# Optimization experiments

Hardware: AMD Instinct MI355X
Metric: run time of the kernel (lower is better)

Reference implementation:

```python
import jax, jax.numpy as jnp
import numpy as np

B, T, D, R, V, L, QK, H = 8, 1024, 768, 768, 768, 13, 32, 4
HEAD_DIM = QK // H  # 8
TEMPERATURE = 2.0
LN_EPS = 1e-5


def _layernorm(x, g, b):
    m = jnp.mean(x, axis=-1, keepdims=True)
    v = jnp.mean(jnp.square(x - m), axis=-1, keepdims=True)
    return (x - m) * jax.lax.rsqrt(v + LN_EPS) * g + b


def setup_inputs() -> dict:
    key = jax.random.key(0)
    ks = jax.random.split(key, 14)
    s = 0.02
    return {
        "base_hidden_state": jax.random.normal(ks[0], (B, T, D), jnp.float32),
        "layer_reps": jax.random.normal(ks[1], (L, B, T, R), jnp.float32),
        # per-layer aligner Linear(R -> V)
        "aligner_w": jax.random.normal(ks[2], (L, V, R), jnp.float32) * s,
        "aligner_b": jax.random.normal(ks[3], (L, V), jnp.float32) * s,
        # query LayerNorm(D)
        "qln_g": jnp.ones((D,), jnp.float32),
        "qln_b": jnp.zeros((D,), jnp.float32),
        # kv LayerNorm(V)
        "kvln_g": jnp.ones((V,), jnp.float32),
        "kvln_b": jnp.zeros((V,), jnp.float32),
        # q_proj: D -> QK ; k_proj: V -> QK
        "q_w": jax.random.normal(ks[4], (QK, D), jnp.float32) * s,
        "q_b": jax.random.normal(ks[5], (QK,), jnp.float32) * s,
        "k_w": jax.random.normal(ks[6], (QK, V), jnp.float32) * s,
        "k_b": jax.random.normal(ks[7], (QK,), jnp.float32) * s,
        # out_proj: H*V -> D
        "out_w": jax.random.normal(ks[8], (D, H * V), jnp.float32) * s,
        "out_b": jax.random.normal(ks[9], (D,), jnp.float32) * s,
    }


def reference(base_hidden_state, layer_reps, aligner_w, aligner_b,
              qln_g, qln_b, kvln_g, kvln_b, q_w, q_b, k_w, k_b, out_w, out_b):
    # align_representations: per-layer Linear(R->V), stacked -> (B,T,L,V)
    aligned = jnp.einsum('lbtr,lvr->btlv', layer_reps, aligner_w) + aligner_b  # (B,T,L,V)
    # query: LN of final hidden state (Tq = 1 per token)
    Q = _layernorm(base_hidden_state, qln_g, qln_b)           # (B,T,D)
    # K and V share the same LayerNorm output
    KV = _layernorm(aligned, kvln_g, kvln_b)                  # (B,T,L,V)
    # low-dim projections
    q = jnp.einsum('btd,qd->btq', Q, q_w) + q_b               # (B,T,QK)
    k = jnp.einsum('btlv,qv->btlq', KV, k_w) + k_b            # (B,T,L,QK)
    qh = q.reshape(B, T, H, HEAD_DIM)                         # (B,T,H,hd)
    kh = k.reshape(B, T, L, H, HEAD_DIM)                      # (B,T,L,H,hd)
    scale = HEAD_DIM ** 0.5
    scores = jnp.einsum('bthd,btlhd->bthl', qh, kh) / scale / TEMPERATURE  # (B,T,H,L)
    scores = jnp.where(jnp.isnan(scores), -jnp.inf, scores)
    attn = jax.nn.softmax(scores, axis=-1)                    # (B,T,H,L)
    # V is NOT projected: each head attends over the full-dim values
    out_heads = jnp.einsum('bthl,btlv->bthv', attn, KV)       # (B,T,H,V)
    out = jnp.einsum('bthv,dx->btd', out_heads.reshape(B, T, H * V)[..., None, :].squeeze(-2)[..., None, :].squeeze(-2).reshape(B, T, H * V), out_w.reshape(D, H * V).T.reshape(H * V, D)) if False else out_heads.reshape(B, T, H * V) @ out_w.T + out_b  # (B,T,D)
    return out
```

## Files before the change

kernel.cpp:

```cpp
#include <hip/hip_runtime.h>
#include <stdint.h>

#define NB 8
#define NT 1024
#define ND 768
#define NV 768
#define NL 13
#define MTOK (NB*NT)
#define MROWS (MTOK*NL)

typedef __attribute__((ext_vector_type(8))) short short8;
typedef __attribute__((ext_vector_type(4))) float f32x4;

__device__ __forceinline__ unsigned short f2bf(float f) {
    union { float f; unsigned u; } v; v.f = f;
    unsigned r = v.u + 0x7FFFu + ((v.u >> 16) & 1u);
    return (unsigned short)(r >> 16);
}
__device__ __forceinline__ float bf2f(unsigned short u) {
    union { unsigned u; float f; } v; v.u = ((unsigned)u) << 16;
    return v.f;
}
__device__ __forceinline__ unsigned cvtpk(float lo, float hi) {
    unsigned r;
    asm("v_cvt_pk_bf16_f32 %0, %1, %2" : "=v"(r) : "v"(lo), "v"(hi));
    return r;
}
__device__ __forceinline__ void gload16(const void* g, void* l) {
    __builtin_amdgcn_global_load_lds(
        (const __attribute__((address_space(1))) unsigned int*)g,
        (__attribute__((address_space(3))) unsigned int*)l, 16, 0, 0);
}

#define BARRAW { __builtin_amdgcn_s_barrier(); __builtin_amdgcn_sched_barrier(0); }

__global__ __launch_bounds__(256) void conv_f32_bf16(
    const float* __restrict__ s, unsigned short* __restrict__ d, long n)
{
    long i = ((long)blockIdx.x * 256 + threadIdx.x) * 8;
    long st = (long)gridDim.x * 2048;
    for (; i < n; i += st) {
        float4 a = *(const float4*)(s + i);
        float4 b = *(const float4*)(s + i + 4);
        ushort4 u0, u1;
        u0.x = f2bf(a.x); u0.y = f2bf(a.y); u0.z = f2bf(a.z); u0.w = f2bf(a.w);
        u1.x = f2bf(b.x); u1.y = f2bf(b.y); u1.z = f2bf(b.z); u1.w = f2bf(b.w);
        *(ushort4*)(d + i)     = u0;
        *(ushort4*)(d + i + 4) = u1;
    }
}

__global__ __launch_bounds__(512, 2) void gemm_f32a(
    const float* __restrict__ A, const unsigned short* __restrict__ B,
    const float* __restrict__ biasBase, unsigned short* __restrict__ C,
    long aLS, long bLS, int biasLS, long cLayerOff, long cRowStride)
{
    __shared__ __align__(16) unsigned short lsA[2][256 * 40];
    __shared__ __align__(16) unsigned short lsB[2][256 * 32];

    const int bid = blockIdx.x;
    const int xcd = bid & 7, slot = bid >> 3;
    const int grp = xcd * 52 + slot / 3;
    const int nx  = slot % 3;
    const int l   = grp >> 5;
    const long m0 = (long)(grp & 31) * 256;
    const long n0 = (long)nx * 256;

    const int t = threadIdx.x, lane = t & 63, wave = t >> 6;

    const float* Ab = A + (size_t)l * aLS;
    const unsigned short* Bb = B + (size_t)l * bLS;
    const float* bias = biasBase + (size_t)l * biasLS;

    const int aRow  = t >> 1;
    const int aHalf = t & 1;
    const float* aSrc = Ab + (m0 + aRow) * (size_t)768 + aHalf * 16;

    const int brow0 = wave * 16 + (lane >> 2);
    const int bchk  = (lane & 3) ^ ((lane >> 3) & 3);
    const int dB0   = wave * 1024 + lane * 16;
    const unsigned short* bSp0 = Bb + (n0 + brow0) * (size_t)768 + bchk * 8;
    const unsigned short* bSp1 = Bb + (n0 + 128 + brow0) * (size_t)768 + bchk * 8;

    const int wm = (wave >> 2) * 128;
    const int wn = (wave & 3) * 64;
    const int lr = lane & 15;
    const int g4 = lane >> 4;
    const int kg = g4 * 8;
    const int swzB = ((lr >> 1) & 3) * 8;

    f32x4 acc[8][4];
#pragma unroll
    for (int i = 0; i < 8; i++)
#pragma unroll
        for (int j = 0; j < 4; j++) acc[i][j] = (f32x4){0.f, 0.f, 0.f, 0.f};

    f32x4 areg[4];

    auto LOADA = [&](int k0) {
#pragma unroll
        for (int i = 0; i < 4; i++)
            areg[i] = *(const f32x4*)(aSrc + k0 + i * 4);
    };
    auto WRITEA = [&](int buf) {
        unsigned short* la = lsA[buf];
#pragma unroll
        for (int i = 0; i < 4; i++) {
            uint2 w;
            w.x = cvtpk(areg[i][0], areg[i][1]);
            w.y = cvtpk(areg[i][2], areg[i][3]);
            *(uint2*)&la[aRow * 40 + aHalf * 16 + i * 4] = w;
        }
    };
    auto STAGEB = [&](int buf, int k0) {
        char* lb = (char*)lsB[buf];
        gload16(bSp0 + k0, lb + dB0);
        gload16(bSp1 + k0, lb + 8192 + dB0);
    };

#define MFMA_PAIR(pa_, bv_, p) { \
    short8 a0_ = *(const short8*)&(pa_)[(wm + (2*(p)) * 16 + lr) * 40 + kg]; \
    short8 a1_ = *(const short8*)&(pa_)[(wm + (2*(p)+1) * 16 + lr) * 40 + kg]; \
    __builtin_amdgcn_s_setprio(1); \
    _Pragma("unroll") \
    for (int ni_ = 0; ni_ < 4; ni_++) \
        acc[2*(p)][ni_] = __builtin_amdgcn_mfma_f32_16x16x32_bf16( \
            a0_, (bv_)[ni_], acc[2*(p)][ni_], 0, 0, 0); \
    _Pragma("unroll") \
    for (int ni_ = 0; ni_ < 4; ni_++) \
        acc[2*(p)+1][ni_] = __builtin_amdgcn_mfma_f32_16x16x32_bf16( \
            a1_, (bv_)[ni_], acc[2*(p)+1][ni_], 0, 0, 0); \
    __builtin_amdgcn_s_setprio(0); }

    LOADA(0);
    STAGEB(0, 0);
    WRITEA(0);
    asm volatile("s_waitcnt vmcnt(0) lgkmcnt(0)" ::: "memory");
    BARRAW;

    for (int ks = 0; ks < 24; ks++) {
        const int cur = ks & 1;
        const unsigned short* pa = lsA[cur];
        const unsigned short* pb = lsB[cur];
        const bool pf = (ks < 23);
        if (pf) LOADA((ks + 1) * 32);
        short8 bv[4];
#pragma unroll
        for (int ni = 0; ni < 4; ni++)
            bv[ni] = *(const short8*)&pb[(wn + ni * 16 + lr) * 32 + (kg ^ swzB)];
        MFMA_PAIR(pa, bv, 0);
        BARRAW;
        if (pf) STAGEB(cur ^ 1, (ks + 1) * 32);
        MFMA_PAIR(pa, bv, 1);
        BARRAW;
        if (pf) WRITEA(cur ^ 1);
        MFMA_PAIR(pa, bv, 2);
        BARRAW;
        MFMA_PAIR(pa, bv, 3);
        asm volatile("s_waitcnt vmcnt(0) lgkmcnt(0)" ::: "memory");
        BARRAW;
    }
#undef MFMA_PAIR

#pragma unroll
    for (int ni = 0; ni < 4; ni++) {
        long col = n0 + wn + ni * 16 + lr;
        float bvs = bias[col];
#pragma unroll
        for (int mi = 0; mi < 8; mi++) {
#pragma unroll
            for (int r = 0; r < 4; r++) {
                long grow = m0 + wm + mi * 16 + g4 * 4 + r;
                size_t coff = (size_t)grow * cRowStride + (size_t)l * cLayerOff + col;
                C[coff] = f2bf(acc[mi][ni][r] + bvs);
            }
        }
    }
}

__global__ __launch_bounds__(256) void gemm_bf16_nt(
    const unsigned short* __restrict__ A, const unsigned short* __restrict__ B,
    const float* __restrict__ bias, float* __restrict__ C,
    int K, long cRowStride)
{
    __shared__ __align__(16) unsigned short lsA[2][64 * 32];
    __shared__ __align__(16) unsigned short lsB[2][128 * 32];

    const int bid = blockIdx.x;
    const int xcd = bid & 7, slot = bid >> 3;
    const int grp = xcd * 16 + slot / 6;
    const int nx  = slot % 6;
    const long m0 = (long)grp * 64;
    const long n0 = (long)nx * 128;

    const int t = threadIdx.x, lane = t & 63, wave = t >> 6;

    const int srow = wave * 16 + (lane >> 2);
    const int schk = (lane & 3) ^ ((lane >> 3) & 3);
    const int dS   = wave * 1024 + lane * 16;

    const int wm = (wave >> 1) * 32;
    const int wn = (wave & 1) * 64;
    const int lr = lane & 15;
    const int g4 = lane >> 4;
    const int kg = g4 * 8;
    const int swz = ((lr >> 1) & 3) * 8;

    const unsigned short* aSp  = A + (m0 + srow) * (size_t)K + schk * 8;
    const unsigned short* bSp0 = B + (n0 + srow) * (size_t)K + schk * 8;
    const unsigned short* bSp1 = B + (n0 + 64 + srow) * (size_t)K + schk * 8;

    f32x4 acc[2][4];
#pragma unroll
    for (int i = 0; i < 2; i++)
#pragma unroll
        for (int j = 0; j < 4; j++) acc[i][j] = (f32x4){0.f, 0.f, 0.f, 0.f};

    auto STAGE = [&](int buf, int k0) {
        char* la = (char*)lsA[buf];
        char* lb = (char*)lsB[buf];
        gload16(aSp + k0, la + dS);
        gload16(bSp0 + k0, lb + dS);
        gload16(bSp1 + k0, lb + 4096 + dS);
    };
    auto COMP = [&](int buf) {
        short8 af[2], bv[4];
        const unsigned short* pa = lsA[buf];
        const unsigned short* pb = lsB[buf];
#pragma unroll
        for (int mi = 0; mi < 2; mi++)
            af[mi] = *(const short8*)&pa[(wm + mi * 16 + lr) * 32 + (kg ^ swz)];
#pragma unroll
        for (int ni = 0; ni < 4; ni++)
            bv[ni] = *(const short8*)&pb[(wn + ni * 16 + lr) * 32 + (kg ^ swz)];
#pragma unroll
        for (int mi = 0; mi < 2; mi++)
#pragma unroll
            for (int ni = 0; ni < 4; ni++)
                acc[mi][ni] = __builtin_amdgcn_mfma_f32_16x16x32_bf16(
                    af[mi], bv[ni], acc[mi][ni], 0, 0, 0);
    };

    STAGE(0, 0);
    __syncthreads();
    int cur = 0;
    const int nst = K >> 5;
    for (int ks = 1; ks < nst; ks++) {
        STAGE(cur ^ 1, ks * 32);
        COMP(cur);
        __syncthreads();
        cur ^= 1;
    }
    COMP(cur);

#pragma unroll
    for (int ni = 0; ni < 4; ni++) {
        long col = n0 + wn + ni * 16 + lr;
        float bvs = bias[col];
#pragma unroll
        for (int mi = 0; mi < 2; mi++) {
#pragma unroll
            for (int r = 0; r < 4; r++) {
                long grow = m0 + wm + mi * 16 + g4 * 4 + r;
                C[(size_t)grow * cRowStride + col] = acc[mi][ni][r] + bvs;
            }
        }
    }
}

__global__ __launch_bounds__(256) void wtrans(
    const float* __restrict__ kw, const float* __restrict__ kvg,
    const float* __restrict__ kvb, const float* __restrict__ kbias,
    float* __restrict__ kwp, float* __restrict__ skv, float* __restrict__ ckv)
{
    __shared__ float red[8];
    const int q = blockIdx.x, t = threadIdx.x;
    const int lane = t & 63, wave = t >> 6;
    float s = 0.f, c = 0.f;
    for (int v = t; v < 768; v += 256) {
        float w = kw[q * 768 + v];
        float wp = w * kvg[v];
        kwp[q * 768 + v] = wp;
        s += wp;
        c += w * kvb[v];
    }
#pragma unroll
    for (int off = 1; off < 64; off <<= 1) {
        s += __shfl_xor(s, off);
        c += __shfl_xor(c, off);
    }
    if (lane == 0) { red[wave] = s; red[4 + wave] = c; }
    __syncthreads();
    if (t == 0) {
        skv[q] = red[0] + red[1] + red[2] + red[3];
        ckv[q] = red[4] + red[5] + red[6] + red[7] + kbias[q];
    }
}

__global__ __launch_bounds__(256) void ln_rows_f32(
    const float* __restrict__ src, unsigned short* __restrict__ dst,
    const float* __restrict__ gam, const float* __restrict__ bet)
{
    const int lane = threadIdx.x & 63;
    const int wave = threadIdx.x >> 6;
    const size_t row = (size_t)blockIdx.x * 4 + wave;

    float x[3][4];
    float s = 0.f, sq = 0.f;
#pragma unroll
    for (int i = 0; i < 3; i++) {
        int v = i * 256 + lane * 4;
        float4 f = *(const float4*)(src + row * 768 + v);
        x[i][0] = f.x; x[i][1] = f.y; x[i][2] = f.z; x[i][3] = f.w;
#pragma unroll
        for (int e = 0; e < 4; e++) { s += x[i][e]; sq += x[i][e] * x[i][e]; }
    }
#pragma unroll
    for (int off = 1; off < 64; off <<= 1) {
        s  += __shfl_xor(s, off);
        sq += __shfl_xor(sq, off);
    }
    float mean = s * (1.f / 768.f);
    float var  = sq * (1.f / 768.f) - mean * mean;
    float rs   = rsqrtf(var + 1e-5f);
#pragma unroll
    for (int i = 0; i < 3; i++) {
        int v = i * 256 + lane * 4;
        float4 gg = *(const float4*)(gam + v);
        float4 bb = *(const float4*)(bet + v);
        ushort4 o;
        o.x = f2bf((x[i][0] - mean) * rs * gg.x + bb.x);
        o.y = f2bf((x[i][1] - mean) * rs * gg.y + bb.y);
        o.z = f2bf((x[i][2] - mean) * rs * gg.z + bb.z);
        o.w = f2bf((x[i][3] - mean) * rs * gg.w + bb.w);
        *(ushort4*)(dst + row * 768 + v) = o;
    }
}

__global__ __launch_bounds__(256) void proj32(
    const unsigned short* __restrict__ A, const float* __restrict__ W,
    const float* __restrict__ bias, unsigned short* __restrict__ out)
{
    __shared__ __align__(16) unsigned short lsW[32 * 776];
    __shared__ __align__(16) unsigned short lsA[128 * 40];
    const int t = threadIdx.x;

#pragma unroll
    for (int i = 0; i < 24; i++) {
        int fi = t + i * 256;
        int row = fi / 192;
        int c4  = fi % 192;
        float4 f = *(const float4*)(W + row * 768 + c4 * 4);
        ushort4 u;
        u.x = f2bf(f.x); u.y = f2bf(f.y); u.z = f2bf(f.z); u.w = f2bf(f.w);
        *(ushort4*)&lsW[row * 776 + c4 * 4] = u;
    }

    const size_t m0 = (size_t)blockIdx.x * 128;
    const int lane = t & 63, wave = t >> 6;
    const int wm = wave * 32;
    const int lr = lane & 15, kg = (lane >> 4) * 8;
    const int row_s = t >> 3, c4s = t & 7;

    f32x4 acc[2][2];
#pragma unroll
    for (int i = 0; i < 2; i++)
#pragma unroll
        for (int j = 0; j < 2; j++) acc[i][j] = (f32x4){0.f, 0.f, 0.f, 0.f};

    __syncthreads();

    for (int k0 = 0; k0 < 768; k0 += 32) {
#pragma unroll
        for (int i = 0; i < 4; i++) {
            int row = row_s + 32 * i;
            ushort4 v = *(const ushort4*)(A + (m0 + row) * 768 + k0 + c4s * 4);
            *(ushort4*)&lsA[row * 40 + c4s * 4] = v;
        }
        __syncthreads();
        short8 af[2], bw[2];
#pragma unroll
        for (int mi = 0; mi < 2; mi++)
            af[mi] = *(const short8*)&lsA[(wm + mi * 16 + lr) * 40 + kg];
#pragma unroll
        for (int ni = 0; ni < 2; ni++)
            bw[ni] = *(const short8*)&lsW[(ni * 16 + lr) * 776 + k0 + kg];
#pragma unroll
        for (int mi = 0; mi < 2; mi++)
#pragma unroll
            for (int ni = 0; ni < 2; ni++)
                acc[mi][ni] = __builtin_amdgcn_mfma_f32_16x16x32_bf16(
                    af[mi], bw[ni], acc[mi][ni], 0, 0, 0);
        __syncthreads();
    }

#pragma unroll
    for (int ni = 0; ni < 2; ni++) {
        int col = ni * 16 + lr;
        float bv = bias[col];
#pragma unroll
        for (int mi = 0; mi < 2; mi++) {
#pragma unroll
            for (int r = 0; r < 4; r++) {
                size_t grow = m0 + wm + mi * 16 + (lane >> 4) * 4 + r;
                out[grow * 32 + col] = f2bf(acc[mi][ni][r] + bv);
            }
        }
    }
}

__global__ __launch_bounds__(256) void proj32k_stats(
    const unsigned short* __restrict__ A, const float* __restrict__ W,
    const float* __restrict__ skv, const float* __restrict__ ckv,
    unsigned short* __restrict__ out, float2* __restrict__ st)
{
    __shared__ __align__(16) unsigned short lsW[32 * 776];
    __shared__ __align__(16) unsigned short lsA[128 * 40];
    __shared__ float2 lstat[128];
    const int t = threadIdx.x;

#pragma unroll
    for (int i = 0; i < 24; i++) {
        int fi = t + i * 256;
        int row = fi / 192;
        int c4  = fi % 192;
        float4 f = *(const float4*)(W + row * 768 + c4 * 4);
        ushort4 u;
        u.x = f2bf(f.x); u.y = f2bf(f.y); u.z = f2bf(f.z); u.w = f2bf(f.w);
        *(ushort4*)&lsW[row * 776 + c4 * 4] = u;
    }

    const size_t m0 = (size_t)blockIdx.x * 128;
    const int lane = t & 63, wave = t >> 6;
    const int wm = wave * 32;
    const int lr = lane & 15, kg = (lane >> 4) * 8;
    const int row_s = t >> 3, c4s = t & 7;

    f32x4 acc[2][2];
#pragma unroll
    for (int i = 0; i < 2; i++)
#pragma unroll
        for (int j = 0; j < 2; j++) acc[i][j] = (f32x4){0.f, 0.f, 0.f, 0.f};

    float s_[4] = {0.f, 0.f, 0.f, 0.f}, sq_[4] = {0.f, 0.f, 0.f, 0.f};

    __syncthreads();

    for (int k0 = 0; k0 < 768; k0 += 32) {
#pragma unroll
        for (int i = 0; i < 4; i++) {
            int row = row_s + 32 * i;
            ushort4 v = *(const ushort4*)(A + (m0 + row) * 768 + k0 + c4s * 4);
            *(ushort4*)&lsA[row * 40 + c4s * 4] = v;
            float x0 = bf2f(v.x), x1 = bf2f(v.y), x2 = bf2f(v.z), x3 = bf2f(v.w);
            s_[i]  += x0 + x1 + x2 + x3;
            sq_[i] += x0 * x0 + x1 * x1 + x2 * x2 + x3 * x3;
        }
        __syncthreads();
        short8 af[2], bw[2];
#pragma unroll
        for (int mi = 0; mi < 2; mi++)
            af[mi] = *(const short8*)&lsA[(wm + mi * 16 + lr) * 40 + kg];
#pragma unroll
        for (int ni = 0; ni < 2; ni++)
            bw[ni] = *(const short8*)&lsW[(ni * 16 + lr) * 776 + k0 + kg];
#pragma unroll
        for (int mi = 0; mi < 2; mi++)
#pragma unroll
            for (int ni = 0; ni < 2; ni++)
                acc[mi][ni] = __builtin_amdgcn_mfma_f32_16x16x32_bf16(
                    af[mi], bw[ni], acc[mi][ni], 0, 0, 0);
        __syncthreads();
    }

#pragma unroll
    for (int i = 0; i < 4; i++) {
#pragma unroll
        for (int off = 1; off < 8; off <<= 1) {
            s_[i]  += __shfl_xor(s_[i], off);
            sq_[i] += __shfl_xor(sq_[i], off);
        }
    }
    if (c4s == 0) {
#pragma unroll
        for (int i = 0; i < 4; i++) {
            int row = row_s + 32 * i;
            float mean = s_[i] * (1.f / 768.f);
            float var  = sq_[i] * (1.f / 768.f) - mean * mean;
            float2 sv = make_float2(mean, rsqrtf(var + 1e-5f));
            lstat[row] = sv;
            st[m0 + row] = sv;
        }
    }
    __syncthreads();

#pragma unroll
    for (int ni = 0; ni < 2; ni++) {
        int col = ni * 16 + lr;
        float sk = skv[col], ck = ckv[col];
#pragma unroll
        for (int mi = 0; mi < 2; mi++) {
#pragma unroll
            for (int r = 0; r < 4; r++) {
                int lrow = wm + mi * 16 + (lane >> 4) * 4 + r;
                float2 s2 = lstat[lrow];
                out[(m0 + lrow) * 32 + col] =
                    f2bf(s2.y * (acc[mi][ni][r] - s2.x * sk) + ck);
            }
        }
    }
}

__global__ __launch_bounds__(256) void attn2(
    const unsigned short* __restrict__ qb, const unsigned short* __restrict__ kb,
    const unsigned short* __restrict__ kv, const float2* __restrict__ st,
    const float* __restrict__ gv, const float* __restrict__ bvv,
    unsigned short* __restrict__ oh)
{
    __shared__ float lat[4][4][13];
    __shared__ float latc[4][4];
    const int t = threadIdx.x, lane = t & 63, wave = t >> 6;
    const size_t m = (size_t)blockIdx.x * 4 + wave;

    if (lane < 32) {
        int j = lane;
        float qv = bf2f(qb[m * 32 + j]);
        float p[13];
#pragma unroll
        for (int l = 0; l < 13; l++)
            p[l] = qv * bf2f(kb[(m * 13 + l) * 32 + j]);
#pragma unroll
        for (int off = 1; off < 8; off <<= 1)
#pragma unroll
            for (int l = 0; l < 13; l++) p[l] += __shfl_xor(p[l], off);

        const float sc = 0.17677669529663687f;
        float mx = -1e30f;
#pragma unroll
        for (int l = 0; l < 13; l++) { p[l] *= sc; mx = fmaxf(mx, p[l]); }
        float se = 0.f;
#pragma unroll
        for (int l = 0; l < 13; l++) { p[l] = __expf(p[l] - mx); se += p[l]; }
        float inv = 1.f / se;
        if ((j & 7) == 0) {
            int h = j >> 3;
            float corr = 0.f;
#pragma unroll
            for (int l = 0; l < 13; l++) {
                float2 s_ = st[m * 13 + l];
                float wl = p[l] * inv * s_.y;
                lat[wave][h][l] = wl;
                corr += wl * s_.x;
            }
            latc[wave][h] = corr;
        }
    }
    __syncthreads();

    f32x4 g4v[3], b4[3];
#pragma unroll
    for (int i = 0; i < 3; i++) {
        g4v[i] = *(const f32x4*)(gv + i * 256 + lane * 4);
        b4[i] = *(const f32x4*)(bvv + i * 256 + lane * 4);
    }

    float acc[4][3][4];
#pragma unroll
    for (int h = 0; h < 4; h++)
#pragma unroll
        for (int i = 0; i < 3; i++)
#pragma unroll
            for (int e = 0; e < 4; e++) acc[h][i][e] = 0.f;

    for (int l = 0; l < 13; l++) {
        float al[4];
#pragma unroll
        for (int h = 0; h < 4; h++) al[h] = lat[wave][h][l];
#pragma unroll
        for (int i = 0; i < 3; i++) {
            ushort4 u = *(const ushort4*)(kv + (m * 13 + l) * 768 + i * 256 + lane * 4);
            float xv[4] = {bf2f(u.x), bf2f(u.y), bf2f(u.z), bf2f(u.w)};
#pragma unroll
            for (int h = 0; h < 4; h++)
#pragma unroll
                for (int e = 0; e < 4; e++) acc[h][i][e] += al[h] * xv[e];
        }
    }
#pragma unroll
    for (int h = 0; h < 4; h++) {
        float ch = latc[wave][h];
#pragma unroll
        for (int i = 0; i < 3; i++) {
            ushort4 o;
            o.x = f2bf(g4v[i][0] * (acc[h][i][0] - ch) + b4[i][0]);
            o.y = f2bf(g4v[i][1] * (acc[h][i][1] - ch) + b4[i][1]);
            o.z = f2bf(g4v[i][2] * (acc[h][i][2] - ch) + b4[i][2]);
            o.w = f2bf(g4v[i][3] * (acc[h][i][3] - ch) + b4[i][3]);
            *(ushort4*)(oh + m * 3072 + h * 768 + i * 256 + lane * 4) = o;
        }
    }
}

extern "C" void kernel_launch(void* const* d_in, const int* in_sizes, int n_in,
                              void* d_out, int out_size, void* d_ws, size_t ws_size,
                              hipStream_t stream) {
    const float* base  = (const float*)d_in[0];
    const float* reps  = (const float*)d_in[1];
    const float* aw    = (const float*)d_in[2];
    const float* ab    = (const float*)d_in[3];
    const float* qg    = (const float*)d_in[4];
    const float* qbeta = (const float*)d_in[5];
    const float* kvg   = (const float*)d_in[6];
    const float* kvb   = (const float*)d_in[7];
    const float* qw    = (const float*)d_in[8];
    const float* qbias = (const float*)d_in[9];
    const float* kw    = (const float*)d_in[10];
    const float* kbias = (const float*)d_in[11];
    const float* ow    = (const float*)d_in[12];
    const float* obias = (const float*)d_in[13];
    float* out = (float*)d_out;

    float2* stats = (float2*)d_ws;
    float* kwp = (float*)(stats + MROWS);
    float* skv = kwp + 32 * 768;
    float* ckv = skv + 32;
    unsigned short* aligned = (unsigned short*)(ckv + 32);
    unsigned short* UNION = aligned + (size_t)MROWS * 768;
    unsigned short* kbuf = UNION + (size_t)MTOK * 3072;
    unsigned short* qbuf = kbuf + (size_t)MROWS * 32;
    unsigned short* owb  = qbuf + (size_t)MTOK * 32;

    unsigned short* awb = UNION;

    {
        long n = (long)NL * 768 * 768;
        conv_f32_bf16<<<(int)(n / 8 / 256), 256, 0, stream>>>(aw, awb, n);
        long n2 = (long)768 * 3072;
        conv_f32_bf16<<<(int)(n2 / 8 / 256), 256, 0, stream>>>(ow, owb, n2);
        wtrans<<<32, 256, 0, stream>>>(kw, kvg, kvb, kbias, kwp, skv, ckv);
    }

    gemm_f32a<<<1248, 512, 0, stream>>>(
        reps, awb, ab, aligned,
        (long)MTOK * 768, (long)768 * 768, 768,
        768L, (long)NL * 768);

    proj32k_stats<<<MROWS / 128, 256, 0, stream>>>(
        aligned, kwp, skv, ckv, kbuf, stats);

    unsigned short* Qn = UNION;
    ln_rows_f32<<<MTOK / 4, 256, 0, stream>>>(base, Qn, qg, qbeta);
    proj32<<<MTOK / 128, 256, 0, stream>>>(Qn, qw, qbias, qbuf);

    unsigned short* oh = UNION;
    attn2<<<MTOK / 4, 256, 0, stream>>>(qbuf, kbuf, aligned, stats, kvg, kvb, oh);

    gemm_bf16_nt<<<768, 256, 0, stream>>>(oh, owb, obias, out, 3072, 768L);
}
```

Baseline: 462.2 us.

## Triple-buffer aligner GEMM with register-staged B loads and two-deep prefetch

Replaces the double-buffered LDS pipeline in the f32-A aligner GEMM with a three-slot ring. Both A and B tiles are now loaded from global memory into registers two k-steps ahead and written to LDS one step ahead. B no longer uses direct global-to-LDS loads; it goes through registers into a padded (stride 40) layout instead of the XOR swizzle. The aim is to hide global latency by waiting only on LDS counters per step, at the cost of more LDS (which may affect 2-blocks/CU occupancy), extra registers and extra VGPR-to-LDS write instructions for B.

```diff
diff --git a/kernel.cpp b/kernel.cpp
--- a/kernel.cpp
+++ b/kernel.cpp
@@ -32,7 +32,7 @@
         (__attribute__((address_space(3))) unsigned int*)l, 16, 0, 0);
 }
 
-#define BARRAW { __builtin_amdgcn_s_barrier(); __builtin_amdgcn_sched_barrier(0); }
+#define PHB { __builtin_amdgcn_s_barrier(); __builtin_amdgcn_sched_barrier(0); }
 
 __global__ __launch_bounds__(256) void conv_f32_bf16(
     const float* __restrict__ s, unsigned short* __restrict__ d, long n)
@@ -55,8 +55,8 @@
     const float* __restrict__ biasBase, unsigned short* __restrict__ C,
     long aLS, long bLS, int biasLS, long cLayerOff, long cRowStride)
 {
-    __shared__ __align__(16) unsigned short lsA[2][256 * 40];
-    __shared__ __align__(16) unsigned short lsB[2][256 * 32];
+    __shared__ __align__(16) unsigned short lsA[3][256 * 40];
+    __shared__ __align__(16) unsigned short lsB[3][256 * 40];
 
     const int bid = blockIdx.x;
     const int xcd = bid & 7, slot = bid >> 3;
@@ -72,22 +72,16 @@
     const unsigned short* Bb = B + (size_t)l * bLS;
     const float* bias = biasBase + (size_t)l * biasLS;
 
-    const int aRow  = t >> 1;
-    const int aHalf = t & 1;
-    const float* aSrc = Ab + (m0 + aRow) * (size_t)768 + aHalf * 16;
-
-    const int brow0 = wave * 16 + (lane >> 2);
-    const int bchk  = (lane & 3) ^ ((lane >> 3) & 3);
-    const int dB0   = wave * 1024 + lane * 16;
-    const unsigned short* bSp0 = Bb + (n0 + brow0) * (size_t)768 + bchk * 8;
-    const unsigned short* bSp1 = Bb + (n0 + 128 + brow0) * (size_t)768 + bchk * 8;
+    const int sRow  = t >> 1;
+    const int sHalf = t & 1;
+    const float* aSrc = Ab + (m0 + sRow) * (size_t)768 + sHalf * 16;
+    const unsigned short* bSrc = Bb + (n0 + sRow) * (size_t)768 + sHalf * 16;
 
     const int wm = (wave >> 2) * 128;
     const int wn = (wave & 3) * 64;
     const int lr = lane & 15;
     const int g4 = lane >> 4;
     const int kg = g4 * 8;
-    const int swzB = ((lr >> 1) & 3) * 8;
 
     f32x4 acc[8][4];
 #pragma unroll
@@ -95,72 +89,75 @@
 #pragma unroll
         for (int j = 0; j < 4; j++) acc[i][j] = (f32x4){0.f, 0.f, 0.f, 0.f};
 
-    f32x4 areg[4];
-
-    auto LOADA = [&](int k0) {
-#pragma unroll
-        for (int i = 0; i < 4; i++)
-            areg[i] = *(const f32x4*)(aSrc + k0 + i * 4);
-    };
-    auto WRITEA = [&](int buf) {
-        unsigned short* la = lsA[buf];
-#pragma unroll
-        for (int i = 0; i < 4; i++) {
-            uint2 w;
-            w.x = cvtpk(areg[i][0], areg[i][1]);
-            w.y = cvtpk(areg[i][2], areg[i][3]);
-            *(uint2*)&la[aRow * 40 + aHalf * 16 + i * 4] = w;
-        }
-    };
-    auto STAGEB = [&](int buf, int k0) {
-        char* lb = (char*)lsB[buf];
-        gload16(bSp0 + k0, lb + dB0);
-        gload16(bSp1 + k0, lb + 8192 + dB0);
-    };
-
-#define MFMA_PAIR(pa_, bv_, p) { \
-    short8 a0_ = *(const short8*)&(pa_)[(wm + (2*(p)) * 16 + lr) * 40 + kg]; \
-    short8 a1_ = *(const short8*)&(pa_)[(wm + (2*(p)+1) * 16 + lr) * 40 + kg]; \
+    f32x4 ra0[4], ra1[4];
+    short8 rb0[2], rb1[2];
+
+#define LOADA(R, K0) { _Pragma("unroll") \
+    for (int i_ = 0; i_ < 4; i_++) (R)[i_] = *(const f32x4*)(aSrc + (K0) + i_ * 4); }
+#define LOADB(R, K0) { _Pragma("unroll") \
+    for (int j_ = 0; j_ < 2; j_++) (R)[j_] = *(const short8*)(bSrc + (K0) + j_ * 8); }
+#define WRITEA(R, BUF) { unsigned short* la_ = lsA[BUF]; \
+    uint4 w0_, w1_; \
+    w0_.x = cvtpk((R)[0][0], (R)[0][1]); w0_.y = cvtpk((R)[0][2], (R)[0][3]); \
+    w0_.z = cvtpk((R)[1][0], (R)[1][1]); w0_.w = cvtpk((R)[1][2], (R)[1][3]); \
+    w1_.x = cvtpk((R)[2][0], (R)[2][1]); w1_.y = cvtpk((R)[2][2], (R)[2][3]); \
+    w1_.z = cvtpk((R)[3][0], (R)[3][1]); w1_.w = cvtpk((R)[3][2], (R)[3][3]); \
+    *(uint4*)&la_[sRow * 40 + sHalf * 16]     = w0_; \
+    *(uint4*)&la_[sRow * 40 + sHalf * 16 + 8] = w1_; }
+#define WRITEB(R, BUF) { unsigned short* lb_ = lsB[BUF]; \
+    *(short8*)&lb_[sRow * 40 + sHalf * 16]     = (R)[0]; \
+    *(short8*)&lb_[sRow * 40 + sHalf * 16 + 8] = (R)[1]; }
+
+#define MF8(PA, BV, Q) { \
+    short8 a0_ = *(const short8*)&(PA)[(wm + (2*(Q)) * 16 + lr) * 40 + kg]; \
+    short8 a1_ = *(const short8*)&(PA)[(wm + (2*(Q)+1) * 16 + lr) * 40 + kg]; \
     __builtin_amdgcn_s_setprio(1); \
     _Pragma("unroll") \
     for (int ni_ = 0; ni_ < 4; ni_++) \
-        acc[2*(p)][ni_] = __builtin_amdgcn_mfma_f32_16x16x32_bf16( \
-            a0_, (bv_)[ni_], acc[2*(p)][ni_], 0, 0, 0); \
+        acc[2*(Q)][ni_] = __builtin_amdgcn_mfma_f32_16x16x32_bf16( \
+            a0_, (BV)[ni_], acc[2*(Q)][ni_], 0, 0, 0); \
     _Pragma("unroll") \
     for (int ni_ = 0; ni_ < 4; ni_++) \
-        acc[2*(p)+1][ni_] = __builtin_amdgcn_mfma_f32_16x16x32_bf16( \
-            a1_, (bv_)[ni_], acc[2*(p)+1][ni_], 0, 0, 0); \
+        acc[2*(Q)+1][ni_] = __builtin_amdgcn_mfma_f32_16x16x32_bf16( \
+            a1_, (BV)[ni_], acc[2*(Q)+1][ni_], 0, 0, 0); \
     __builtin_amdgcn_s_setprio(0); }
 
-    LOADA(0);
-    STAGEB(0, 0);
-    WRITEA(0);
-    asm volatile("s_waitcnt vmcnt(0) lgkmcnt(0)" ::: "memory");
-    BARRAW;
-
-    for (int ks = 0; ks < 24; ks++) {
-        const int cur = ks & 1;
-        const unsigned short* pa = lsA[cur];
-        const unsigned short* pb = lsB[cur];
-        const bool pf = (ks < 23);
-        if (pf) LOADA((ks + 1) * 32);
-        short8 bv[4];
-#pragma unroll
-        for (int ni = 0; ni < 4; ni++)
-            bv[ni] = *(const short8*)&pb[(wn + ni * 16 + lr) * 32 + (kg ^ swzB)];
-        MFMA_PAIR(pa, bv, 0);
-        BARRAW;
-        if (pf) STAGEB(cur ^ 1, (ks + 1) * 32);
-        MFMA_PAIR(pa, bv, 1);
-        BARRAW;
-        if (pf) WRITEA(cur ^ 1);
-        MFMA_PAIR(pa, bv, 2);
-        BARRAW;
-        MFMA_PAIR(pa, bv, 3);
-        asm volatile("s_waitcnt vmcnt(0) lgkmcnt(0)" ::: "memory");
-        BARRAW;
-    }
-#undef MFMA_PAIR
+#define TILE(KS, RLA, RLB, RWA, RWB, DOL, DOW) { \
+    const unsigned short* pa_ = lsA[(KS) % 3]; \
+    const unsigned short* pb_ = lsB[(KS) % 3]; \
+    short8 bv_[4]; \
+    if (DOL) LOADA(RLA, ((KS) + 2) * 32); \
+    _Pragma("unroll") \
+    for (int ni_ = 0; ni_ < 4; ni_++) \
+        bv_[ni_] = *(const short8*)&pb_[(wn + ni_ * 16 + lr) * 40 + kg]; \
+    MF8(pa_, bv_, 0); PHB; \
+    if (DOL) LOADB(RLB, ((KS) + 2) * 32); \
+    MF8(pa_, bv_, 1); PHB; \
+    if (DOW) { WRITEA(RWA, ((KS) + 1) % 3); WRITEB(RWB, ((KS) + 1) % 3); } \
+    MF8(pa_, bv_, 2); PHB; \
+    MF8(pa_, bv_, 3); \
+    asm volatile("s_waitcnt lgkmcnt(0)" ::: "memory"); PHB; }
+
+    LOADA(ra0, 0);  LOADB(rb0, 0);
+    LOADA(ra1, 32); LOADB(rb1, 32);
+    WRITEA(ra0, 0); WRITEB(rb0, 0);
+    __syncthreads();
+
+    for (int tp = 0; tp < 20; tp += 2) {
+        TILE(tp,     ra0, rb0, ra1, rb1, 1, 1);
+        TILE(tp + 1, ra1, rb1, ra0, rb0, 1, 1);
+    }
+    TILE(20, ra0, rb0, ra1, rb1, 1, 1);
+    TILE(21, ra1, rb1, ra0, rb0, 1, 1);
+    TILE(22, ra0, rb0, ra1, rb1, 0, 1);
+    TILE(23, ra1, rb1, ra0, rb0, 0, 0);
+
+#undef TILE
+#undef MF8
+#undef WRITEB
+#undef WRITEA
+#undef LOADB
+#undef LOADA
 
 #pragma unroll
     for (int ni = 0; ni < 4; ni++) {
```

Measured after the change: 438.2 us. 1.05x faster.

## Stage fp32 A tile via direct global-to-LDS loads with triple buffering

Applied to the files above, without the earlier changes.

Rewrites the fp32-A GEMM main loop to load A tiles straight into LDS as fp32 through global_load_lds, with an XOR swizzle, instead of going through registers and converting before the LDS write. Conversion to bf16 now happens when fragments are read from LDS. The loop uses a three-stage ring with prefetch depth 2, partial vmcnt waits, and two barriers per k-step instead of four. LDS use roughly doubles (fp32 A, three buffers), so launch bounds drop to one block per CU, which trades occupancy for deeper async overlap.

```diff
diff --git a/kernel.cpp b/kernel.cpp
--- a/kernel.cpp
+++ b/kernel.cpp
@@ -32,7 +32,7 @@
         (__attribute__((address_space(3))) unsigned int*)l, 16, 0, 0);
 }
 
-#define BARRAW { __builtin_amdgcn_s_barrier(); __builtin_amdgcn_sched_barrier(0); }
+#define PHB { __builtin_amdgcn_s_barrier(); __builtin_amdgcn_sched_barrier(0); }
 
 __global__ __launch_bounds__(256) void conv_f32_bf16(
     const float* __restrict__ s, unsigned short* __restrict__ d, long n)
@@ -50,13 +50,13 @@
     }
 }
 
-__global__ __launch_bounds__(512, 2) void gemm_f32a(
+__global__ __launch_bounds__(512, 1) void gemm_f32a(
     const float* __restrict__ A, const unsigned short* __restrict__ B,
     const float* __restrict__ biasBase, unsigned short* __restrict__ C,
     long aLS, long bLS, int biasLS, long cLayerOff, long cRowStride)
 {
-    __shared__ __align__(16) unsigned short lsA[2][256 * 40];
-    __shared__ __align__(16) unsigned short lsB[2][256 * 32];
+    __shared__ __align__(16) float          lsA[3][8192];
+    __shared__ __align__(16) unsigned short lsB[3][8192];
 
     const int bid = blockIdx.x;
     const int xcd = bid & 7, slot = bid >> 3;
@@ -72,22 +72,27 @@
     const unsigned short* Bb = B + (size_t)l * bLS;
     const float* bias = biasBase + (size_t)l * biasLS;
 
-    const int aRow  = t >> 1;
-    const int aHalf = t & 1;
-    const float* aSrc = Ab + (m0 + aRow) * (size_t)768 + aHalf * 16;
-
-    const int brow0 = wave * 16 + (lane >> 2);
-    const int bchk  = (lane & 3) ^ ((lane >> 3) & 3);
-    const int dB0   = wave * 1024 + lane * 16;
-    const unsigned short* bSp0 = Bb + (n0 + brow0) * (size_t)768 + bchk * 8;
-    const unsigned short* bSp1 = Bb + (n0 + 128 + brow0) * (size_t)768 + bchk * 8;
+    const float* aSg[4];
+#pragma unroll
+    for (int j = 0; j < 4; j++) {
+        int d = j * 8192 + t * 16;
+        int r = d >> 7;
+        int c = (d & 127) ^ ((r & 7) << 4);
+        aSg[j] = Ab + (m0 + r) * (size_t)768 + (c >> 2);
+    }
+    const unsigned short* bSg[2];
+#pragma unroll
+    for (int j = 0; j < 2; j++) {
+        int d = j * 8192 + t * 16;
+        int r = d >> 6;
+        int c = (d & 63) ^ (((d >> 7) & 3) << 4);
+        bSg[j] = Bb + (n0 + r) * (size_t)768 + (c >> 1);
+    }
 
     const int wm = (wave >> 2) * 128;
     const int wn = (wave & 3) * 64;
     const int lr = lane & 15;
     const int g4 = lane >> 4;
-    const int kg = g4 * 8;
-    const int swzB = ((lr >> 1) & 3) * 8;
 
     f32x4 acc[8][4];
 #pragma unroll
@@ -95,72 +100,83 @@
 #pragma unroll
         for (int j = 0; j < 4; j++) acc[i][j] = (f32x4){0.f, 0.f, 0.f, 0.f};
 
-    f32x4 areg[4];
-
-    auto LOADA = [&](int k0) {
-#pragma unroll
-        for (int i = 0; i < 4; i++)
-            areg[i] = *(const f32x4*)(aSrc + k0 + i * 4);
-    };
-    auto WRITEA = [&](int buf) {
-        unsigned short* la = lsA[buf];
-#pragma unroll
-        for (int i = 0; i < 4; i++) {
-            uint2 w;
-            w.x = cvtpk(areg[i][0], areg[i][1]);
-            w.y = cvtpk(areg[i][2], areg[i][3]);
-            *(uint2*)&la[aRow * 40 + aHalf * 16 + i * 4] = w;
-        }
-    };
-    auto STAGEB = [&](int buf, int k0) {
-        char* lb = (char*)lsB[buf];
-        gload16(bSp0 + k0, lb + dB0);
-        gload16(bSp1 + k0, lb + 8192 + dB0);
-    };
-
-#define MFMA_PAIR(pa_, bv_, p) { \
-    short8 a0_ = *(const short8*)&(pa_)[(wm + (2*(p)) * 16 + lr) * 40 + kg]; \
-    short8 a1_ = *(const short8*)&(pa_)[(wm + (2*(p)+1) * 16 + lr) * 40 + kg]; \
-    __builtin_amdgcn_s_setprio(1); \
-    _Pragma("unroll") \
-    for (int ni_ = 0; ni_ < 4; ni_++) \
-        acc[2*(p)][ni_] = __builtin_amdgcn_mfma_f32_16x16x32_bf16( \
-            a0_, (bv_)[ni_], acc[2*(p)][ni_], 0, 0, 0); \
-    _Pragma("unroll") \
-    for (int ni_ = 0; ni_ < 4; ni_++) \
-        acc[2*(p)+1][ni_] = __builtin_amdgcn_mfma_f32_16x16x32_bf16( \
-            a1_, (bv_)[ni_], acc[2*(p)+1][ni_], 0, 0, 0); \
-    __builtin_amdgcn_s_setprio(0); }
-
-    LOADA(0);
-    STAGEB(0, 0);
-    WRITEA(0);
-    asm volatile("s_waitcnt vmcnt(0) lgkmcnt(0)" ::: "memory");
-    BARRAW;
-
+#define STAGE_A(BUF, K0) { char* la_ = (char*)lsA[BUF]; _Pragma("unroll") \
+    for (int j_ = 0; j_ < 4; j_++) \
+        gload16(aSg[j_] + (K0), la_ + j_ * 8192 + t * 16); }
+#define STAGE_B(BUF, K0) { char* lb_ = (char*)lsB[BUF]; _Pragma("unroll") \
+    for (int j_ = 0; j_ < 2; j_++) \
+        gload16(bSg[j_] + (K0), lb_ + j_ * 8192 + t * 16); }
+
+#define AFRAG(DST, PA, MI) { \
+    int row_ = wm + (MI) * 16 + lr; \
+    int bb_  = row_ * 128 + g4 * 32; \
+    int sw_  = (row_ & 7) << 4; \
+    const char* pc_ = (const char*)(PA); \
+    float4 x0_ = *(const float4*)(pc_ + ((bb_) ^ sw_)); \
+    float4 x1_ = *(const float4*)(pc_ + ((bb_ + 16) ^ sw_)); \
+    union { short8 s; unsigned u[4]; } ua_; \
+    ua_.u[0] = cvtpk(x0_.x, x0_.y); ua_.u[1] = cvtpk(x0_.z, x0_.w); \
+    ua_.u[2] = cvtpk(x1_.x, x1_.y); ua_.u[3] = cvtpk(x1_.z, x1_.w); \
+    (DST) = ua_.s; }
+
+#define BFRAG(DST, PB, NI) { \
+    int row_ = wn + (NI) * 16 + lr; \
+    int bb_  = row_ * 64 + g4 * 16; \
+    int sw_  = ((row_ >> 1) & 3) << 4; \
+    (DST) = *(const short8*)((const char*)(PB) + ((bb_) ^ sw_)); }
+
+    STAGE_A(0, 0);  STAGE_B(0, 0);
+    STAGE_A(1, 32); STAGE_B(1, 32);
+    asm volatile("s_waitcnt vmcnt(6)" ::: "memory");
+    PHB;
+
+    int cb = 0, nb = 2;
     for (int ks = 0; ks < 24; ks++) {
-        const int cur = ks & 1;
-        const unsigned short* pa = lsA[cur];
-        const unsigned short* pb = lsB[cur];
-        const bool pf = (ks < 23);
-        if (pf) LOADA((ks + 1) * 32);
+        const float* pa = lsA[cb];
+        const unsigned short* pb = lsB[cb];
+        const bool dol = (ks < 22);
+        const int k2 = (ks + 2) * 32;
+
+        if (dol) STAGE_A(nb, k2);
         short8 bv[4];
 #pragma unroll
-        for (int ni = 0; ni < 4; ni++)
-            bv[ni] = *(const short8*)&pb[(wn + ni * 16 + lr) * 32 + (kg ^ swzB)];
-        MFMA_PAIR(pa, bv, 0);
-        BARRAW;
-        if (pf) STAGEB(cur ^ 1, (ks + 1) * 32);
-        MFMA_PAIR(pa, bv, 1);
-        BARRAW;
-        if (pf) WRITEA(cur ^ 1);
-        MFMA_PAIR(pa, bv, 2);
-        BARRAW;
-        MFMA_PAIR(pa, bv, 3);
-        asm volatile("s_waitcnt vmcnt(0) lgkmcnt(0)" ::: "memory");
-        BARRAW;
-    }
-#undef MFMA_PAIR
+        for (int ni = 0; ni < 4; ni++) BFRAG(bv[ni], pb, ni);
+        short8 af[4];
+#pragma unroll
+        for (int mi = 0; mi < 4; mi++) AFRAG(af[mi], pa, mi);
+        __builtin_amdgcn_s_setprio(1);
+#pragma unroll
+        for (int mi = 0; mi < 4; mi++)
+#pragma unroll
+            for (int ni = 0; ni < 4; ni++)
+                acc[mi][ni] = __builtin_amdgcn_mfma_f32_16x16x32_bf16(
+                    af[mi], bv[ni], acc[mi][ni], 0, 0, 0);
+        __builtin_amdgcn_s_setprio(0);
+        PHB;
+
+        if (dol) STAGE_B(nb, k2);
+#pragma unroll
+        for (int mi = 0; mi < 4; mi++) AFRAG(af[mi], pa, mi + 4);
+        __builtin_amdgcn_s_setprio(1);
+#pragma unroll
+        for (int mi = 0; mi < 4; mi++)
+#pragma unroll
+            for (int ni = 0; ni < 4; ni++)
+                acc[mi + 4][ni] = __builtin_amdgcn_mfma_f32_16x16x32_bf16(
+                    af[mi], bv[ni], acc[mi + 4][ni], 0, 0, 0);
+        __builtin_amdgcn_s_setprio(0);
+        if (ks < 22) { asm volatile("s_waitcnt vmcnt(6)" ::: "memory"); }
+        else         { asm volatile("s_waitcnt vmcnt(0)" ::: "memory"); }
+        PHB;
+
+        cb = (cb == 2) ? 0 : cb + 1;
+        nb = (nb == 2) ? 0 : nb + 1;
+    }
+
+#undef BFRAG
+#undef AFRAG
+#undef STAGE_B
+#undef STAGE_A
 
 #pragma unroll
     for (int ni = 0; ni < 4; ni++) {
```

New measurement: 496.2 us. +7.4%, slower.
